# Performance work log

Measured on AMD Instinct MI355X. Metric: run time of the kernel, lower is better.

Reference implementation:

```python
import jax, jax.numpy as jnp
import numpy as np

C = 256
C8 = C // 8  # query/key channels

def setup_inputs() -> dict:
    key = jax.random.key(0)
    ks = jax.random.split(key, 8)
    B, H, W = 8, 64, 64
    s = 1.0 / np.sqrt(C)
    x  = jax.random.normal(ks[0], (B, C, H, W), dtype=jnp.float32)
    Wq = jax.random.normal(ks[1], (C8, C), dtype=jnp.float32) * s
    bq = jax.random.normal(ks[2], (C8,), dtype=jnp.float32) * 0.01
    Wk = jax.random.normal(ks[3], (C8, C), dtype=jnp.float32) * s
    bk = jax.random.normal(ks[4], (C8,), dtype=jnp.float32) * 0.01
    Wv = jax.random.normal(ks[5], (C, C), dtype=jnp.float32) * s
    bv = jax.random.normal(ks[6], (C,), dtype=jnp.float32) * 0.01
    gamma = jnp.zeros((1,), dtype=jnp.float32) + 0.5  # nonzero so output depends on attention
    return {"x": x, "Wq": Wq, "bq": bq, "Wk": Wk, "bk": bk, "Wv": Wv, "bv": bv, "gamma": gamma}

def reference(x, Wq, bq, Wk, bk, Wv, bv, gamma):
    B, Cc, H, W = x.shape
    N = H * W
    xf = x.reshape(B, Cc, N)                      # [B,C,N]
    # 1x1 convs == channel matmuls
    q = jnp.einsum('dc,bcn->bdn', Wq, xf) + bq[None, :, None]   # [B,C8,N]
    k = jnp.einsum('dc,bcn->bdn', Wk, xf) + bk[None, :, None]   # [B,C8,N]
    v = jnp.einsum('dc,bcn->bdn', Wv, xf) + bv[None, :, None]   # [B,C,N]
    # attention[b,n,m] = sum_d q[b,d,n] * k[b,d,m]
    attn = jnp.einsum('bdn,bdm->bnm', q, k)       # [B,N,N]
    attn = jax.nn.softmax(attn, axis=-1)
    # out[b,c,n] = sum_m v[b,c,m] * attn[b,n,m]
    out = jnp.einsum('bcm,bnm->bcn', v, attn).reshape(B, Cc, H, W)
    return gamma[0] * out + x
```

## Files before the change

### kernel.cpp

```cpp
#include <hip/hip_runtime.h>
#include <hip/hip_bf16.h>

#define C_DIM 256
#define C8 32
#define N_DIM 4096
#define B_DIM 8
#define KSTEPS 64

using bf16x8 = __attribute__((ext_vector_type(8))) __bf16;
using f32x4  = __attribute__((ext_vector_type(4))) float;
using f32x16 = __attribute__((ext_vector_type(16))) float;
using uint2v = __attribute__((ext_vector_type(2))) unsigned;

#define LOG2E 1.44269504088896f


__global__ __launch_bounds__(256) void k_qkv(
    const float* __restrict__ x,
    const float* __restrict__ Wq, const float* __restrict__ bq,
    const float* __restrict__ Wk, const float* __restrict__ bk,
    const float* __restrict__ Wv, const float* __restrict__ bv,
    __bf16* __restrict__ Qt, __bf16* __restrict__ Kt, __bf16* __restrict__ Vb)
{
    __shared__ __align__(16) float  tile[64][65];
    __shared__ __align__(16) __bf16 xs[64][264];

    int bid = blockIdx.x;
    int b   = bid & 7;
    int nt  = bid >> 3;
    int n0  = nt * 64;
    int t   = threadIdx.x;

    const float* xb = x + (size_t)b * C_DIM * N_DIM;
#pragma unroll
    for (int ct = 0; ct < 4; ct++) {
        int c0 = ct * 64;
#pragma unroll
        for (int k = 0; k < 16; k++) {
            int idx = k * 256 + t;
            int i = idx >> 6, j = idx & 63;
            tile[i][j] = xb[(size_t)(c0 + i) * N_DIM + n0 + j];
        }
        __syncthreads();
#pragma unroll
        for (int k = 0; k < 16; k++) {
            int idx = k * 256 + t;
            int nl = idx >> 6, cl = idx & 63;
            xs[nl][c0 + cl] = (__bf16)tile[cl][nl];
        }
        __syncthreads();
    }

    int wid = t >> 6, lane = t & 63;
    int lg = lane >> 4, li = lane & 15;

    __bf16* Qtb = Qt + (size_t)b * (N_DIM * 32);
    __bf16* Ktb = Kt + (size_t)b * (N_DIM * 32);
    __bf16* Vtb = Vb + (size_t)b * (N_DIM * C_DIM);

#pragma unroll
    for (int dt = 0; dt < 5; dt++) {
        int d0w = dt * 64 + wid * 16;
        int drow = d0w + li;
        const float* wrow;
        if (drow < 32)        wrow = Wq + drow * C_DIM;
        else if (drow < 64)   wrow = Wk + (drow - 32) * C_DIM;
        else                  wrow = Wv + (drow - 64) * C_DIM;

        f32x4 acc[4] = {};
#pragma unroll
        for (int ksx = 0; ksx < 8; ksx++) {
            int c0 = ksx * 32 + lg * 8;
            float4 w0 = *(const float4*)(wrow + c0);
            float4 w1 = *(const float4*)(wrow + c0 + 4);
            bf16x8 af;
            af[0] = (__bf16)w0.x; af[1] = (__bf16)w0.y;
            af[2] = (__bf16)w0.z; af[3] = (__bf16)w0.w;
            af[4] = (__bf16)w1.x; af[5] = (__bf16)w1.y;
            af[6] = (__bf16)w1.z; af[7] = (__bf16)w1.w;
#pragma unroll
            for (int ns = 0; ns < 4; ns++) {
                bf16x8 bfr = *(const bf16x8*)(&xs[ns * 16 + li][ksx * 32 + lg * 8]);
                acc[ns] = __builtin_amdgcn_mfma_f32_16x16x32_bf16(af, bfr, acc[ns], 0, 0, 0);
            }
        }
#pragma unroll
        for (int r = 0; r < 4; r++) {
            int d = d0w + lg * 4 + r;
            float bias = (d < 32) ? bq[d] : (d < 64) ? bk[d - 32] : bv[d - 64];
#pragma unroll
            for (int ns = 0; ns < 4; ns++) {
                int n = n0 + ns * 16 + li;
                float v = acc[ns][r] + bias;
                if (d < 32) {
                    int dd = d;
                    Qtb[((n >> 5) << 10) + ((dd >> 3) << 8) + ((n & 31) << 3) + (dd & 7)]
                        = (__bf16)(v * LOG2E);
                } else if (d < 64) {
                    int dd = d - 32;
                    Ktb[((n >> 5) << 10) + ((dd >> 3) << 8) + ((n & 31) << 3) + (dd & 7)]
                        = (__bf16)v;
                } else {
                    int c = d - 64;
                    Vtb[((n >> 4) << 12) + (((n >> 3) & 1) << 11) + (c << 3) + (n & 7)]
                        = (__bf16)v;
                }
            }
        }
    }
}

static __device__ __forceinline__ unsigned pack2(float a, float b) {
    union { __bf16 h[2]; unsigned u; } c;
    c.h[0] = (__bf16)a; c.h[1] = (__bf16)b; return c.u;
}
static __device__ __forceinline__ bf16x8 mkfrag(unsigned d0, unsigned d1, unsigned d2, unsigned d3) {
    union { unsigned u[4]; bf16x8 v; } r;
    r.u[0] = d0; r.u[1] = d1; r.u[2] = d2; r.u[3] = d3; return r.v;
}
static __device__ __forceinline__ uint2v plswap(unsigned a, unsigned b) {
#if __has_builtin(__builtin_amdgcn_permlane32_swap)
    return __builtin_amdgcn_permlane32_swap(a, b, false, false);
#else
    unsigned ax = (unsigned)__shfl_xor((int)a, 32);
    unsigned bx = (unsigned)__shfl_xor((int)b, 32);
    int hi = (threadIdx.x >> 5) & 1;
    uint2v r;
    r.x = hi ? bx : a;
    r.y = hi ? b  : ax;
    return r;
#endif
}
static __device__ __forceinline__ void soft_pack(
    const f32x16& s, float& l, bf16x8& f0, bf16x8& f1)
{
    float p[16];
#pragma unroll
    for (int r = 0; r < 16; r++) p[r] = __builtin_amdgcn_exp2f(s[r]);
    float lp = 0.f;
#pragma unroll
    for (int r = 0; r < 16; r++) lp += p[r];
    l += lp;
    unsigned a0 = pack2(p[0],  p[1]),  b0 = pack2(p[2],  p[3]);
    unsigned a1 = pack2(p[4],  p[5]),  b1 = pack2(p[6],  p[7]);
    unsigned a2 = pack2(p[8],  p[9]),  b2 = pack2(p[10], p[11]);
    unsigned a3 = pack2(p[12], p[13]), b3 = pack2(p[14], p[15]);
    uint2v rA0 = plswap(a0, a1), rB0 = plswap(b0, b1);
    uint2v rA1 = plswap(a2, a3), rB1 = plswap(b2, b3);
    f0 = mkfrag(rA0.x, rB0.x, rA0.y, rB0.y);
    f1 = mkfrag(rA1.x, rB1.x, rA1.y, rB1.y);
}

__global__ __launch_bounds__(256, 2) void k_attn(
    const __bf16* __restrict__ Qt, const __bf16* __restrict__ Kt,
    const __bf16* __restrict__ Vb, const float* __restrict__ x,
    const float* __restrict__ gamma, float* __restrict__ out)
{
    __shared__ __bf16 accs[2][C_DIM][32];
    __shared__ float  lbuf[2][32];

    int bid = blockIdx.x;
    int b   = bid & 7;
    int qp  = bid >> 3;
    int wid  = threadIdx.x >> 6;
    int qsel = wid >> 1;
    int ks   = wid & 1;
    int li  = threadIdx.x & 31;
    int hi  = (threadIdx.x >> 5) & 1;
    int n0q = (qp * 2 + qsel) * 32;

    const __bf16* Qtb = Qt + (size_t)b * (N_DIM * 32);
    const __bf16* Ktb = Kt + (size_t)b * (N_DIM * 32);
    const __bf16* Vtb = Vb + (size_t)b * (N_DIM * C_DIM);

    const __bf16* Qlp = Qtb + ((n0q >> 5) << 10) + (hi << 8) + (li << 3);
    bf16x8 qf0 = *(const bf16x8*)(Qlp);
    bf16x8 qf1 = *(const bf16x8*)(Qlp + 512);

    const __bf16* Klp = Ktb + ((size_t)(ks * KSTEPS) << 10) + (hi << 8) + (li << 3);
    const __bf16* Vlp = Vtb + ((size_t)(ks * KSTEPS) << 13) + (hi << 11) + (li << 3);

    f32x16 acc0 = {}, acc1 = {}, acc2 = {}, acc3 = {};
    f32x16 acc4 = {}, acc5 = {}, acc6 = {}, acc7 = {};
    float l0 = 0.f;

    bf16x8 kA0, kA1, kB0, kB1;

#define KLOAD(D0, D1, S)                                                       \
    { const __bf16* Kn = Klp + ((size_t)(S) << 10);                            \
      D0 = *(const bf16x8*)(Kn); D1 = *(const bf16x8*)(Kn + 512); }

#define STEP(KU0, KU1, KL0, KL1, KS2, I)                                       \
    {                                                                          \
        f32x16 z = {};                                                         \
        f32x16 s = __builtin_amdgcn_mfma_f32_32x32x16_bf16(KU0, qf0, z, 0, 0, 0); \
        s = __builtin_amdgcn_mfma_f32_32x32x16_bf16(KU1, qf1, s, 0, 0, 0);     \
        KLOAD(KL0, KL1, KS2)                                                   \
        const __bf16* Vn = Vlp + ((size_t)(I) << 13);                          \
        bf16x8 v0 = *(const bf16x8*)(Vn);                                      \
        bf16x8 v1 = *(const bf16x8*)(Vn + 4096);                               \
        bf16x8 v2 = *(const bf16x8*)(Vn + 256);                                \
        bf16x8 v3 = *(const bf16x8*)(Vn + 4096 + 256);                         \
        bf16x8 v4 = *(const bf16x8*)(Vn + 512);                                \
        bf16x8 v5 = *(const bf16x8*)(Vn + 4096 + 512);                         \
        bf16x8 v6 = *(const bf16x8*)(Vn + 768);                                \
        bf16x8 v7 = *(const bf16x8*)(Vn + 4096 + 768);                         \
        bf16x8 p0, p1;                                                         \
        soft_pack(s, l0, p0, p1);                                              \
        acc0 = __builtin_amdgcn_mfma_f32_32x32x16_bf16(v0, p0, acc0, 0, 0, 0); \
        acc0 = __builtin_amdgcn_mfma_f32_32x32x16_bf16(v1, p1, acc0, 0, 0, 0); \
        bf16x8 w0 = *(const bf16x8*)(Vn + 1024);                               \
        bf16x8 w1 = *(const bf16x8*)(Vn + 4096 + 1024);                        \
        acc1 = __builtin_amdgcn_mfma_f32_32x32x16_bf16(v2, p0, acc1, 0, 0, 0); \
        acc1 = __builtin_amdgcn_mfma_f32_32x32x16_bf16(v3, p1, acc1, 0, 0, 0); \
        bf16x8 w2 = *(const bf16x8*)(Vn + 1280);                               \
        bf16x8 w3 = *(const bf16x8*)(Vn + 4096 + 1280);                        \
        acc2 = __builtin_amdgcn_mfma_f32_32x32x16_bf16(v4, p0, acc2, 0, 0, 0); \
        acc2 = __builtin_amdgcn_mfma_f32_32x32x16_bf16(v5, p1, acc2, 0, 0, 0); \
        bf16x8 w4 = *(const bf16x8*)(Vn + 1536);                               \
        bf16x8 w5 = *(const bf16x8*)(Vn + 4096 + 1536);                        \
        acc3 = __builtin_amdgcn_mfma_f32_32x32x16_bf16(v6, p0, acc3, 0, 0, 0); \
        acc3 = __builtin_amdgcn_mfma_f32_32x32x16_bf16(v7, p1, acc3, 0, 0, 0); \
        bf16x8 w6 = *(const bf16x8*)(Vn + 1792);                               \
        bf16x8 w7 = *(const bf16x8*)(Vn + 4096 + 1792);                        \
        acc4 = __builtin_amdgcn_mfma_f32_32x32x16_bf16(w0, p0, acc4, 0, 0, 0); \
        acc4 = __builtin_amdgcn_mfma_f32_32x32x16_bf16(w1, p1, acc4, 0, 0, 0); \
        acc5 = __builtin_amdgcn_mfma_f32_32x32x16_bf16(w2, p0, acc5, 0, 0, 0); \
        acc5 = __builtin_amdgcn_mfma_f32_32x32x16_bf16(w3, p1, acc5, 0, 0, 0); \
        acc6 = __builtin_amdgcn_mfma_f32_32x32x16_bf16(w4, p0, acc6, 0, 0, 0); \
        acc6 = __builtin_amdgcn_mfma_f32_32x32x16_bf16(w5, p1, acc6, 0, 0, 0); \
        acc7 = __builtin_amdgcn_mfma_f32_32x32x16_bf16(w6, p0, acc7, 0, 0, 0); \
        acc7 = __builtin_amdgcn_mfma_f32_32x32x16_bf16(w7, p1, acc7, 0, 0, 0); \
    }

    KLOAD(kA0, kA1, 0)
    KLOAD(kB0, kB1, 1)

    for (int i = 0; i < KSTEPS - 2; i += 2) {
        STEP(kA0, kA1, kA0, kA1, i + 2, i)
        STEP(kB0, kB1, kB0, kB1, i + 3, i + 1)
    }
    STEP(kA0, kA1, kA0, kA1, KSTEPS - 1, KSTEPS - 2)
    STEP(kB0, kB1, kB0, kB1, KSTEPS - 1, KSTEPS - 1)

#undef STEP
#undef KLOAD

    float lv = l0 + __shfl_xor(l0, 32);

    if (ks == 1) {
        if (hi == 0) lbuf[qsel][li] = lv;
#define SPILL_ACC(A, G)                                                        \
        _Pragma("unroll")                                                      \
        for (int rg = 0; rg < 16; rg++) {                                      \
            int row = (rg & 3) + 8 * (rg >> 2) + 4 * hi;                       \
            accs[qsel][(G) * 32 + row][li] = (__bf16)A[rg];                    \
        }
        SPILL_ACC(acc0, 0) SPILL_ACC(acc1, 1) SPILL_ACC(acc2, 2) SPILL_ACC(acc3, 3)
        SPILL_ACC(acc4, 4) SPILL_ACC(acc5, 5) SPILL_ACC(acc6, 6) SPILL_ACC(acc7, 7)
#undef SPILL_ACC
    }
    __syncthreads();
    if (ks == 0) {
        float lt = lv + lbuf[qsel][li];
        float linv = gamma[0] / lt;
#define STORE_ACC(A, G)                                                        \
        _Pragma("unroll")                                                      \
        for (int rg = 0; rg < 16; rg++) {                                      \
            int row = (rg & 3) + 8 * (rg >> 2) + 4 * hi;                       \
            int c = (G) * 32 + row;                                            \
            size_t idx = ((size_t)b * C_DIM + c) * N_DIM + (n0q + li);         \
            float o = A[rg] + (float)accs[qsel][c][li];                        \
            out[idx] = o * linv + x[idx];                                      \
        }
        STORE_ACC(acc0, 0) STORE_ACC(acc1, 1) STORE_ACC(acc2, 2) STORE_ACC(acc3, 3)
        STORE_ACC(acc4, 4) STORE_ACC(acc5, 5) STORE_ACC(acc6, 6) STORE_ACC(acc7, 7)
#undef STORE_ACC
    }
}

extern "C" void kernel_launch(void* const* d_in, const int* in_sizes, int n_in,
                              void* d_out, int out_size, void* d_ws, size_t ws_size,
                              hipStream_t stream)
{
    const float* x     = (const float*)d_in[0];
    const float* Wq    = (const float*)d_in[1];
    const float* bq    = (const float*)d_in[2];
    const float* Wk    = (const float*)d_in[3];
    const float* bk    = (const float*)d_in[4];
    const float* Wv    = (const float*)d_in[5];
    const float* bv    = (const float*)d_in[6];
    const float* gamma = (const float*)d_in[7];
    float* out = (float*)d_out;

    char* ws = (char*)d_ws;
    const size_t MB = 1024 * 1024;
    __bf16* Qt = (__bf16*)ws;
    __bf16* Kt = (__bf16*)(ws + 2 * MB);
    __bf16* Vb = (__bf16*)(ws + 4 * MB);

    k_qkv<<<512, 256, 0, stream>>>(x, Wq, bq, Wk, bk, Wv, bv, Qt, Kt, Vb);
    k_attn<<<512, 256, 0, stream>>>(Qt, Kt, Vb, x, gamma, out);
}
```

Before: 131.7 us.

## Stage V tiles into double-buffered LDS with async global-to-LDS loads

V tiles, which were read directly from global memory in each step, are now prefetched one step ahead into double-buffered shared memory using global_load_lds. The two waves that share a K-split each stage half of the tile, so V is loaded once per block and shared between the two query waves instead of being fetched by each. A __syncthreads is added after every step, and the V buffer is reused afterwards for the accumulator spill. The intent is to halve redundant V traffic and overlap the loads with MFMA work, at the cost of per-step barriers and 64KB of LDS, which may limit occupancy at 2 blocks per CU.

```diff
diff --git a/kernel.cpp b/kernel.cpp
--- a/kernel.cpp
+++ b/kernel.cpp
@@ -151,13 +151,20 @@
     f1 = mkfrag(rA1.x, rB1.x, rA1.y, rB1.y);
 }
 
+static __device__ __forceinline__ void gload_lds16(const __bf16* g, __bf16* l) {
+    __builtin_amdgcn_global_load_lds(
+        (const __attribute__((address_space(1))) unsigned int*)(g),
+        (__attribute__((address_space(3))) unsigned int*)(l),
+        16, 0, 0);
+}
+
 __global__ __launch_bounds__(256, 2) void k_attn(
     const __bf16* __restrict__ Qt, const __bf16* __restrict__ Kt,
     const __bf16* __restrict__ Vb, const float* __restrict__ x,
     const float* __restrict__ gamma, float* __restrict__ out)
 {
-    __shared__ __bf16 accs[2][C_DIM][32];
-    __shared__ float  lbuf[2][32];
+    __shared__ __align__(16) __bf16 smV[2][2][8192];
+    __shared__ float lbuf[2][32];
 
     int bid = blockIdx.x;
     int b   = bid & 7;
@@ -165,6 +172,7 @@
     int wid  = threadIdx.x >> 6;
     int qsel = wid >> 1;
     int ks   = wid & 1;
+    int lane = threadIdx.x & 63;
     int li  = threadIdx.x & 31;
     int hi  = (threadIdx.x >> 5) & 1;
     int n0q = (qp * 2 + qsel) * 32;
@@ -178,7 +186,9 @@
     bf16x8 qf1 = *(const bf16x8*)(Qlp + 512);
 
     const __bf16* Klp = Ktb + ((size_t)(ks * KSTEPS) << 10) + (hi << 8) + (li << 3);
-    const __bf16* Vlp = Vtb + ((size_t)(ks * KSTEPS) << 13) + (hi << 11) + (li << 3);
+
+    __bf16* vbufA = &smV[ks][0][0];
+    __bf16* vbufB = &smV[ks][1][0];
 
     f32x16 acc0 = {}, acc1 = {}, acc2 = {}, acc3 = {};
     f32x16 acc4 = {}, acc5 = {}, acc6 = {}, acc7 = {};
@@ -190,13 +200,22 @@
     { const __bf16* Kn = Klp + ((size_t)(S) << 10);                            \
       D0 = *(const bf16x8*)(Kn); D1 = *(const bf16x8*)(Kn + 512); }
 
-#define STEP(KU0, KU1, KL0, KL1, KS2, I)                                       \
+#define STAGE(VST, S)                                                          \
+    { const __bf16* gs = Vtb + (((size_t)(ks * KSTEPS + (S))) << 13)           \
+                         + qsel * 4096 + (lane << 3);                          \
+      __bf16* ld = (VST) + qsel * 4096;                                        \
+      _Pragma("unroll")                                                        \
+      for (int j = 0; j < 8; j++)                                              \
+          gload_lds16(gs + j * 512, ld + j * 512); }
+
+#define STEP(KU0, KU1, KL0, KL1, KS2, I, VRD, VST)                             \
     {                                                                          \
+        if ((I) + 1 < KSTEPS) STAGE(VST, (I) + 1)                              \
         f32x16 z = {};                                                         \
         f32x16 s = __builtin_amdgcn_mfma_f32_32x32x16_bf16(KU0, qf0, z, 0, 0, 0); \
         s = __builtin_amdgcn_mfma_f32_32x32x16_bf16(KU1, qf1, s, 0, 0, 0);     \
         KLOAD(KL0, KL1, KS2)                                                   \
-        const __bf16* Vn = Vlp + ((size_t)(I) << 13);                          \
+        const __bf16* Vn = (VRD) + (hi << 11) + (li << 3);                     \
         bf16x8 v0 = *(const bf16x8*)(Vn);                                      \
         bf16x8 v1 = *(const bf16x8*)(Vn + 4096);                               \
         bf16x8 v2 = *(const bf16x8*)(Vn + 256);                                \
@@ -231,21 +250,26 @@
         acc6 = __builtin_amdgcn_mfma_f32_32x32x16_bf16(w5, p1, acc6, 0, 0, 0); \
         acc7 = __builtin_amdgcn_mfma_f32_32x32x16_bf16(w6, p0, acc7, 0, 0, 0); \
         acc7 = __builtin_amdgcn_mfma_f32_32x32x16_bf16(w7, p1, acc7, 0, 0, 0); \
-    }
-
+        __syncthreads();                                                       \
+    }
+
+    STAGE(vbufA, 0)
     KLOAD(kA0, kA1, 0)
     KLOAD(kB0, kB1, 1)
+    __syncthreads();
 
     for (int i = 0; i < KSTEPS - 2; i += 2) {
-        STEP(kA0, kA1, kA0, kA1, i + 2, i)
-        STEP(kB0, kB1, kB0, kB1, i + 3, i + 1)
-    }
-    STEP(kA0, kA1, kA0, kA1, KSTEPS - 1, KSTEPS - 2)
-    STEP(kB0, kB1, kB0, kB1, KSTEPS - 1, KSTEPS - 1)
+        STEP(kA0, kA1, kA0, kA1, i + 2, i,     vbufA, vbufB)
+        STEP(kB0, kB1, kB0, kB1, i + 3, i + 1, vbufB, vbufA)
+    }
+    STEP(kA0, kA1, kA0, kA1, KSTEPS - 1, KSTEPS - 2, vbufA, vbufB)
+    STEP(kB0, kB1, kB0, kB1, KSTEPS - 1, KSTEPS - 1, vbufB, vbufA)
 
 #undef STEP
+#undef STAGE
 #undef KLOAD
 
+    __bf16 (*accs)[C_DIM][32] = (__bf16 (*)[C_DIM][32])(&smV[0][0][0]);
     float lv = l0 + __shfl_xor(l0, 32);
 
     if (ks == 1) {
```

Measured after the change: 131.7 us. Within noise of the previous version (+0.0%).
